# Optimization experiments

Hardware: AMD Instinct MI355X
Metric: run time of the kernel (lower is better)

## Reference

```python
import jax, jax.numpy as jnp
import numpy as np

B, N, D, H = 8, 1024, 1024, 16
HD = D // H  # head_size = 64


def setup_inputs() -> dict:
    key = jax.random.key(0)
    k0, k1, k2, k3, k4 = jax.random.split(key, 5)
    scale = 1.0 / np.sqrt(D)
    return {
        "x": jax.random.normal(k0, (B, N, D), dtype=jnp.float32),
        "Wqkv": jax.random.normal(k1, (D, 3 * D), dtype=jnp.float32) * scale,
        "bqkv": jnp.zeros((3 * D,), dtype=jnp.float32),
        "Wo": jax.random.normal(k2, (D, D), dtype=jnp.float32) * scale,
        "bo": jnp.zeros((D,), dtype=jnp.float32),
    }


def reference(x, Wqkv, bqkv, Wo, bo):
    # Fused QKV projection: [B, N, 3D]
    qkv = jnp.einsum("bnd,de->bne", x, Wqkv) + bqkv
    q, k, v = jnp.split(qkv, 3, axis=-1)

    def split_heads(t):  # [B, N, D] -> [B, H, N, HD]
        return t.reshape(B, N, H, HD).transpose(0, 2, 1, 3)

    q, k, v = split_heads(q), split_heads(k), split_heads(v)

    # Scaled dot-product attention (no mask, dropout=0)
    scores = jnp.einsum("bhqd,bhkd->bhqk", q, k) / jnp.sqrt(jnp.float32(HD))
    alpha = jax.nn.softmax(scores, axis=-1)
    ctx = jnp.einsum("bhqk,bhkd->bhqd", alpha, v)  # [B, H, N, HD]

    ctx = ctx.transpose(0, 2, 1, 3).reshape(B, N, D)
    out = jnp.einsum("bnd,de->bne", ctx, Wo) + bo
    return out
```

## Files before the change

kernel.cpp:

```cpp
#include <hip/hip_runtime.h>
#include <cstdint>
#include <cstddef>

typedef _Float16 half_t;
typedef __attribute__((ext_vector_type(4))) _Float16 half4v;
typedef __attribute__((ext_vector_type(8))) _Float16 half8v;
typedef __attribute__((ext_vector_type(4))) float float4v;
typedef __attribute__((ext_vector_type(16))) float float16v;
typedef __attribute__((ext_vector_type(4))) unsigned uint4v;
typedef __attribute__((ext_vector_type(2))) int int2v;

typedef __attribute__((address_space(1))) const void gv_t;
typedef __attribute__((address_space(3))) void lv_t;

__device__ __forceinline__ void lds_cp16(const void* g, void* l) {
  __builtin_amdgcn_global_load_lds((gv_t*)g, (lv_t*)l, 16, 0, 0);
}

__device__ __forceinline__ unsigned pkh(float a, float b) {
  return __builtin_bit_cast(unsigned, __builtin_amdgcn_cvt_pkrtz(a, b));
}

__global__ __launch_bounds__(256) void k_cvt(const float* __restrict__ in,
                                             half_t* __restrict__ out) {
  int i = blockIdx.x * 256 + threadIdx.x;
  float4 v = ((const float4*)in)[i];
  half4v h = {(half_t)v.x, (half_t)v.y, (half_t)v.z, (half_t)v.w};
  ((half4v*)out)[i] = h;
}

__global__ __launch_bounds__(256) void k_tcvt(const float* __restrict__ in,
                                              half_t* __restrict__ out, int R, int C) {
  __shared__ float t[32][33];
  int c0 = blockIdx.x * 32, r0 = blockIdx.y * 32;
  int tc = threadIdx.x & 31, tr = threadIdx.x >> 5;
#pragma unroll
  for (int i = 0; i < 4; i++)
    t[tr + i * 8][tc] = in[(size_t)(r0 + tr + i * 8) * C + c0 + tc];
  __syncthreads();
#pragma unroll
  for (int i = 0; i < 4; i++)
    out[(size_t)(c0 + tr + i * 8) * R + r0 + tc] = (half_t)t[tc][tr + i * 8];
}

template <int EPI>
__global__ __launch_bounds__(256, 2) void k_gemm(
    const half_t* __restrict__ A, const half_t* __restrict__ Bt,
    const float* __restrict__ bias, float* __restrict__ Cout,
    half_t* __restrict__ Qo, half_t* __restrict__ Ko, half_t* __restrict__ Vo,
    int M, int N, int K) {
  __shared__ half_t As[2][128 * 64];
  __shared__ half_t Bs[2][128 * 64];
  const int tid = threadIdx.x;
  const int lane = tid & 63;
  const int w = tid >> 6;
  const int xcd = blockIdx.x & 7;
  const int l = blockIdx.x >> 3;
  const int nc = l >> 6, r = l & 63;
  const int m0 = (xcd * 8 + (r >> 3)) * 128;
  const int n0 = (nc * 8 + (r & 7)) * 128;
  const int wr = w >> 1, wc = w & 1;

  int sr[4];
  int sg[4];
#pragma unroll
  for (int j = 0; j < 4; ++j) {
    const int G = j * 256 + tid;
    sr[j] = G >> 3;
    sg[j] = (G & 7) ^ (sr[j] & 7);
  }

  float4v acc[4][4] = {};

  const int fr = lane & 15;
  const int fg = lane >> 4;
  const int so0 = ((0 << 2) | fg) ^ (fr & 7);
  const int so1 = ((1 << 2) | fg) ^ (fr & 7);
  const int arow = wr * 64 + fr;
  const int brow = wc * 64 + fr;

  const int NT = K >> 6;
#pragma unroll
  for (int j = 0; j < 4; ++j) {
    lds_cp16(A + (size_t)(m0 + sr[j]) * K + sg[j] * 8, &As[0][(j * 256 + tid) * 8]);
    lds_cp16(Bt + (size_t)(n0 + sr[j]) * K + sg[j] * 8, &Bs[0][(j * 256 + tid) * 8]);
  }

  for (int t = 0; t < NT; t++) {
    asm volatile("s_waitcnt vmcnt(0)" ::: "memory");
    __builtin_amdgcn_s_barrier();
    __builtin_amdgcn_sched_barrier(0);
    const int cb = t & 1;
    if (t + 1 < NT) {
      const int kn = (t + 1) * 64;
#pragma unroll
      for (int j = 0; j < 4; ++j) {
        lds_cp16(A + (size_t)(m0 + sr[j]) * K + kn + sg[j] * 8,
                 &As[cb ^ 1][(j * 256 + tid) * 8]);
        lds_cp16(Bt + (size_t)(n0 + sr[j]) * K + kn + sg[j] * 8,
                 &Bs[cb ^ 1][(j * 256 + tid) * 8]);
      }
    }
    half8v a[4][2], b[4][2];
#pragma unroll
    for (int m = 0; m < 4; m++) {
      const int row = (arow + m * 16) * 64;
      a[m][0] = *(const half8v*)(&As[cb][row + so0 * 8]);
      a[m][1] = *(const half8v*)(&As[cb][row + so1 * 8]);
    }
#pragma unroll
    for (int n = 0; n < 4; n++) {
      const int row = (brow + n * 16) * 64;
      b[n][0] = *(const half8v*)(&Bs[cb][row + so0 * 8]);
      b[n][1] = *(const half8v*)(&Bs[cb][row + so1 * 8]);
    }
    __builtin_amdgcn_s_setprio(1);
#pragma unroll
    for (int kk = 0; kk < 2; kk++)
#pragma unroll
      for (int m = 0; m < 4; m++)
#pragma unroll
        for (int n = 0; n < 4; n++)
          acc[m][n] = __builtin_amdgcn_mfma_f32_16x16x32_f16(a[m][kk], b[n][kk],
                                                             acc[m][n], 0, 0, 0);
    __builtin_amdgcn_s_setprio(0);
  }

  const int rq = (lane >> 4) * 4;
  const int cc = lane & 15;
  if constexpr (EPI == 0) {
#pragma unroll
    for (int n = 0; n < 4; n++) {
      int e = n0 + wc * 64 + n * 16 + cc;
      float bv = bias[e];
      int which = e >> 10, h = (e >> 6) & 15, hd = e & 63;
#pragma unroll
      for (int m = 0; m < 4; m++) {
        int rowb = m0 + wr * 64 + m * 16 + rq;
#pragma unroll
        for (int r2 = 0; r2 < 4; r2++) {
          int row = rowb + r2;
          int b_ = row >> 10, tok = row & 1023;
          half_t hv = (half_t)(acc[m][n][r2] + bv);
          size_t bh = (size_t)(b_ * 16 + h);
          if (which == 0)
            Qo[(bh * 1024 + tok) * 64 + hd] = hv;
          else if (which == 1)
            Ko[(bh * 1024 + tok) * 64 + hd] = hv;
          else
            Vo[(bh * 64 + hd) * 1024 + tok] = hv;
        }
      }
    }
  } else {
#pragma unroll
    for (int n = 0; n < 4; n++) {
      int e = n0 + wc * 64 + n * 16 + cc;
      float bv = bias[e];
#pragma unroll
      for (int m = 0; m < 4; m++) {
        int rowb = m0 + wr * 64 + m * 16 + rq;
#pragma unroll
        for (int r2 = 0; r2 < 4; r2++)
          Cout[(size_t)(rowb + r2) * N + e] = acc[m][n][r2] + bv;
      }
    }
  }
}

__global__ __launch_bounds__(512, 4) void k_attn(const half_t* __restrict__ Qh,
                                                 const half_t* __restrict__ Kh,
                                                 const half_t* __restrict__ Vt,
                                                 half_t* __restrict__ ctx) {
  __shared__ alignas(16) half_t Ks[2][64 * 64];
  __shared__ alignas(16) half_t Vs[2][64 * 64];
  const int lane = threadIdx.x & 63;
  const int w = threadIdx.x >> 6;
  const int ql = lane & 31, hi = lane >> 5;
  const int xcd = blockIdx.x & 7, loc = blockIdx.x >> 3;
  const int bh = xcd * 16 + (loc >> 2), qb = loc & 3;
  const int b_ = bh >> 4, h = bh & 15;
  const int q0 = qb * 256 + w * 32;

  const half_t* Qp = Qh + (size_t)bh * (1024 * 64);
  const half_t* Kp = Kh + (size_t)bh * (1024 * 64);
  const half_t* Vp = Vt + (size_t)bh * (64 * 1024);

  half8v qf[4];
#pragma unroll
  for (int c = 0; c < 4; c++) {
    half8v tq = *(const half8v*)(Qp + (size_t)(q0 + ql) * 64 + c * 16 + hi * 8);
    qf[c] = tq * (_Float16)0.125f;
  }

  const int G = w * 64 + lane;
  const int rS = G >> 3;
  const int gS = (G & 7) ^ (rS & 7);

  float16v co[2] = {};
  float mr = -1e30f, ssum = 0.f;

  lds_cp16(Kp + (size_t)rS * 64 + gS * 8, &Ks[0][w * 512]);
  lds_cp16(Vp + (size_t)rS * 1024 + 0 + gS * 8, &Vs[0][w * 512]);
  __syncthreads();

  int cur = 0;
  for (int t = 0; t < 16; t++) {
    if (t < 15) {
      const int kn = (t + 1) * 64;
      lds_cp16(Kp + (size_t)(kn + rS) * 64 + gS * 8, &Ks[cur ^ 1][w * 512]);
      lds_cp16(Vp + (size_t)rS * 1024 + kn + gS * 8, &Vs[cur ^ 1][w * 512]);
    }

    float16v sacc[2] = {};
    __builtin_amdgcn_s_setprio(1);
#pragma unroll
    for (int c = 0; c < 4; c++)
#pragma unroll
      for (int s = 0; s < 2; s++) {
        int row = s * 32 + ql;
        half8v kf = *(const half8v*)(&Ks[cur][row * 64 + (((2 * c + hi) ^ (row & 7)) * 8)]);
        sacc[s] = __builtin_amdgcn_mfma_f32_32x32x16_f16(kf, qf[c], sacc[s], 0, 0, 0);
      }
    __builtin_amdgcn_s_setprio(0);

    float mx = -1e30f;
#pragma unroll
    for (int s = 0; s < 2; s++)
#pragma unroll
      for (int i = 0; i < 16; i++) mx = fmaxf(mx, sacc[s][i]);
    mx = fmaxf(mx, __shfl_xor(mx, 32, 64));
    if (mx > mr + 8.f) {
      float fac = __expf(mr - mx);
      mr = mx;
      ssum *= fac;
#pragma unroll
      for (int dd = 0; dd < 2; dd++)
#pragma unroll
        for (int i = 0; i < 16; i++) co[dd][i] *= fac;
    }
    float rsum = 0.f;
#pragma unroll
    for (int s = 0; s < 2; s++)
#pragma unroll
      for (int i = 0; i < 16; i++) {
        float e = __expf(sacc[s][i] - mr);
        sacc[s][i] = e;
        rsum += e;
      }
    rsum += __shfl_xor(rsum, 32, 64);
    ssum += rsum;

#pragma unroll
    for (int kc = 0; kc < 4; kc++) {
      const int s = kc >> 1, o = (kc & 1) * 8;
      unsigned dA0 = pkh(sacc[s][o + 0], sacc[s][o + 1]);
      unsigned dA1 = pkh(sacc[s][o + 2], sacc[s][o + 3]);
      unsigned dB0 = pkh(sacc[s][o + 4], sacc[s][o + 5]);
      unsigned dB1 = pkh(sacc[s][o + 6], sacc[s][o + 7]);
      int2v r0 = __builtin_amdgcn_permlane32_swap((int)dA0, (int)dB0, false, false);
      int2v r1 = __builtin_amdgcn_permlane32_swap((int)dA1, (int)dB1, false, false);
      uint4v pw = {(unsigned)r0.x, (unsigned)r1.x, (unsigned)r0.y, (unsigned)r1.y};
      half8v pf = __builtin_bit_cast(half8v, pw);
      __builtin_amdgcn_s_setprio(1);
#pragma unroll
      for (int dd = 0; dd < 2; dd++) {
        int row = dd * 32 + ql;
        half8v vf = *(const half8v*)(&Vs[cur][row * 64 + (((2 * kc + hi) ^ (row & 7)) * 8)]);
        co[dd] = __builtin_amdgcn_mfma_f32_32x32x16_f16(vf, pf, co[dd], 0, 0, 0);
      }
      __builtin_amdgcn_s_setprio(0);
    }
    __syncthreads();
    cur ^= 1;
  }

  float rinv = 1.0f / ssum;
  half_t* outp = ctx + ((size_t)(b_ * 1024 + q0 + ql) * 1024 + h * 64);
#pragma unroll
  for (int dd = 0; dd < 2; dd++)
#pragma unroll
    for (int g = 0; g < 4; g++) {
      int d0 = dd * 32 + g * 8 + hi * 4;
      unsigned p0 = pkh(co[dd][g * 4 + 0] * rinv, co[dd][g * 4 + 1] * rinv);
      unsigned p1 = pkh(co[dd][g * 4 + 2] * rinv, co[dd][g * 4 + 3] * rinv);
      *(unsigned*)(outp + d0) = p0;
      *(unsigned*)(outp + d0 + 2) = p1;
    }
}

extern "C" void kernel_launch(void* const* d_in, const int* in_sizes, int n_in,
                              void* d_out, int out_size, void* d_ws, size_t ws_size,
                              hipStream_t stream) {
  const float* x = (const float*)d_in[0];
  const float* Wqkv = (const float*)d_in[1];
  const float* bqkv = (const float*)d_in[2];
  const float* Wo = (const float*)d_in[3];
  const float* bo = (const float*)d_in[4];
  float* out = (float*)d_out;
  char* ws = (char*)d_ws;

  const size_t NEED = 75497472;
  if (ws_size < NEED) return;
  half_t* xh = (half_t*)(ws);
  half_t* wqkvT = (half_t*)(ws + 16777216);
  half_t* woT = (half_t*)(ws + 23068672);
  half_t* Qh = (half_t*)(ws + 25165824);
  half_t* Kh = (half_t*)(ws + 41943040);
  half_t* Vt = (half_t*)(ws + 58720256);
  half_t* ctxh = xh;

  k_cvt<<<8192, 256, 0, stream>>>(x, xh);
  k_tcvt<<<dim3(96, 32), 256, 0, stream>>>(Wqkv, wqkvT, 1024, 3072);
  k_tcvt<<<dim3(32, 32), 256, 0, stream>>>(Wo, woT, 1024, 1024);
  k_gemm<0><<<1536, 256, 0, stream>>>(xh, wqkvT, bqkv, nullptr, Qh, Kh, Vt,
                                      8192, 3072, 1024);
  k_attn<<<512, 512, 0, stream>>>(Qh, Kh, Vt, ctxh);
  k_gemm<1><<<512, 256, 0, stream>>>(ctxh, woT, bo, out, nullptr, nullptr, nullptr,
                                     8192, 1024, 1024);
}
```

Before: 171.3 us.

## Load QKV GEMM A operand directly to registers, halving LDS footprint

```diff
diff --git a/kernel.cpp b/kernel.cpp
--- a/kernel.cpp
+++ b/kernel.cpp
@@ -43,12 +43,111 @@
     out[(size_t)(c0 + tr + i * 8) * R + r0 + tc] = (half_t)t[tc][tr + i * 8];
 }
 
-template <int EPI>
-__global__ __launch_bounds__(256, 2) void k_gemm(
+__global__ __launch_bounds__(256, 3) void k_qkv(
     const half_t* __restrict__ A, const half_t* __restrict__ Bt,
-    const float* __restrict__ bias, float* __restrict__ Cout,
-    half_t* __restrict__ Qo, half_t* __restrict__ Ko, half_t* __restrict__ Vo,
-    int M, int N, int K) {
+    const float* __restrict__ bias,
+    half_t* __restrict__ Qo, half_t* __restrict__ Ko, half_t* __restrict__ Vo) {
+  __shared__ half_t Bs[2][128 * 64];
+  const int tid = threadIdx.x;
+  const int lane = tid & 63;
+  const int w = tid >> 6;
+  const int xcd = blockIdx.x & 7;
+  const int l = blockIdx.x >> 3;
+  const int nc = l >> 6, r = l & 63;
+  const int m0 = (xcd * 8 + (r >> 3)) * 128;
+  const int n0 = (nc * 8 + (r & 7)) * 128;
+  const int wr = w >> 1, wc = w & 1;
+  const int fr = lane & 15, fg = lane >> 4;
+
+  int sr[4], sg[4];
+#pragma unroll
+  for (int j = 0; j < 4; ++j) {
+    const int G = j * 256 + tid;
+    sr[j] = G >> 3;
+    sg[j] = (G & 7) ^ (sr[j] & 7);
+  }
+
+  const half_t* Ap = A + (size_t)(m0 + wr * 64 + fr) * 1024 + fg * 8;
+
+  float4v acc[4][4] = {};
+  const int so0 = fg ^ (fr & 7);
+  const int so1 = (4 | fg) ^ (fr & 7);
+  const int brow = wc * 64 + fr;
+
+  half8v a0[8], a1[8];
+#pragma unroll
+  for (int j = 0; j < 4; ++j)
+    lds_cp16(Bt + (size_t)(n0 + sr[j]) * 1024 + sg[j] * 8, &Bs[0][(j * 256 + tid) * 8]);
+#pragma unroll
+  for (int m = 0; m < 4; ++m)
+#pragma unroll
+    for (int kk = 0; kk < 2; ++kk)
+      a0[m * 2 + kk] = *(const half8v*)(Ap + m * 16384 + kk * 32);
+  asm volatile("s_waitcnt vmcnt(0)" ::: "memory");
+  __builtin_amdgcn_s_barrier();
+
+#define QKV_ITER(t, cb, ac, an)                                                  \
+  do {                                                                           \
+    if ((t) + 1 < 16) {                                                          \
+      const int kn = ((t) + 1) * 64;                                             \
+      _Pragma("unroll") for (int j = 0; j < 4; ++j)                              \
+          lds_cp16(Bt + (size_t)(n0 + sr[j]) * 1024 + kn + sg[j] * 8,            \
+                   &Bs[(cb) ^ 1][(j * 256 + tid) * 8]);                          \
+      _Pragma("unroll") for (int m = 0; m < 4; ++m)                              \
+          _Pragma("unroll") for (int kk = 0; kk < 2; ++kk)                       \
+              an[m * 2 + kk] = *(const half8v*)(Ap + m * 16384 + kn + kk * 32);  \
+    }                                                                            \
+    _Pragma("unroll") for (int kk = 0; kk < 2; ++kk) {                           \
+      half8v b[4];                                                               \
+      _Pragma("unroll") for (int n = 0; n < 4; ++n) {                            \
+        const int row = (brow + n * 16) * 64;                                    \
+        b[n] = *(const half8v*)(&Bs[cb][row + (kk ? so1 : so0) * 8]);            \
+      }                                                                          \
+      _Pragma("unroll") for (int m = 0; m < 4; ++m)                              \
+          _Pragma("unroll") for (int n = 0; n < 4; ++n)                          \
+              acc[m][n] = __builtin_amdgcn_mfma_f32_16x16x32_f16(                \
+                  ac[m * 2 + kk], b[n], acc[m][n], 0, 0, 0);                     \
+    }                                                                            \
+    asm volatile("s_waitcnt vmcnt(0)" ::: "memory");                             \
+    __builtin_amdgcn_s_barrier();                                                \
+  } while (0)
+
+  for (int tp = 0; tp < 8; ++tp) {
+    QKV_ITER(2 * tp, 0, a0, a1);
+    QKV_ITER(2 * tp + 1, 1, a1, a0);
+  }
+#undef QKV_ITER
+
+  const int rq = (lane >> 4) * 4;
+  const int cc = lane & 15;
+#pragma unroll
+  for (int n = 0; n < 4; n++) {
+    const int e = n0 + wc * 64 + n * 16 + cc;
+    const float bv = bias[e];
+    const int which = e >> 10, h = (e >> 6) & 15, hd = e & 63;
+#pragma unroll
+    for (int m = 0; m < 4; m++) {
+      const int rowb = m0 + wr * 64 + m * 16 + rq;
+#pragma unroll
+      for (int r2 = 0; r2 < 4; r2++) {
+        const int row = rowb + r2;
+        const int b_ = row >> 10, tok = row & 1023;
+        const half_t hv = (half_t)(acc[m][n][r2] + bv);
+        const size_t bh = (size_t)(b_ * 16 + h);
+        if (which == 0)
+          Qo[(bh * 1024 + tok) * 64 + hd] = hv;
+        else if (which == 1)
+          Ko[(bh * 1024 + tok) * 64 + hd] = hv;
+        else
+          Vo[(bh * 64 + hd) * 1024 + tok] = hv;
+      }
+    }
+  }
+}
+
+__global__ __launch_bounds__(256, 2) void k_gemm_o(
+    const half_t* __restrict__ A, const half_t* __restrict__ Bt,
+    const float* __restrict__ bias, float* __restrict__ Cout, int N, int K) {
   __shared__ half_t As[2][128 * 64];
   __shared__ half_t Bs[2][128 * 64];
   const int tid = threadIdx.x;
@@ -61,8 +160,7 @@
   const int n0 = (nc * 8 + (r & 7)) * 128;
   const int wr = w >> 1, wc = w & 1;
 
-  int sr[4];
-  int sg[4];
+  int sr[4], sg[4];
 #pragma unroll
   for (int j = 0; j < 4; ++j) {
     const int G = j * 256 + tid;
@@ -71,11 +169,10 @@
   }
 
   float4v acc[4][4] = {};
-
   const int fr = lane & 15;
   const int fg = lane >> 4;
-  const int so0 = ((0 << 2) | fg) ^ (fr & 7);
-  const int so1 = ((1 << 2) | fg) ^ (fr & 7);
+  const int so0 = fg ^ (fr & 7);
+  const int so1 = (4 | fg) ^ (fr & 7);
   const int arow = wr * 64 + fr;
   const int brow = wc * 64 + fr;
 
@@ -114,7 +211,6 @@
       b[n][0] = *(const half8v*)(&Bs[cb][row + so0 * 8]);
       b[n][1] = *(const half8v*)(&Bs[cb][row + so1 * 8]);
     }
-    __builtin_amdgcn_s_setprio(1);
 #pragma unroll
     for (int kk = 0; kk < 2; kk++)
 #pragma unroll
@@ -123,47 +219,20 @@
         for (int n = 0; n < 4; n++)
           acc[m][n] = __builtin_amdgcn_mfma_f32_16x16x32_f16(a[m][kk], b[n][kk],
                                                              acc[m][n], 0, 0, 0);
-    __builtin_amdgcn_s_setprio(0);
   }
 
   const int rq = (lane >> 4) * 4;
   const int cc = lane & 15;
-  if constexpr (EPI == 0) {
-#pragma unroll
-    for (int n = 0; n < 4; n++) {
-      int e = n0 + wc * 64 + n * 16 + cc;
-      float bv = bias[e];
-      int which = e >> 10, h = (e >> 6) & 15, hd = e & 63;
-#pragma unroll
-      for (int m = 0; m < 4; m++) {
-        int rowb = m0 + wr * 64 + m * 16 + rq;
-#pragma unroll
-        for (int r2 = 0; r2 < 4; r2++) {
-          int row = rowb + r2;
-          int b_ = row >> 10, tok = row & 1023;
-          half_t hv = (half_t)(acc[m][n][r2] + bv);
-          size_t bh = (size_t)(b_ * 16 + h);
-          if (which == 0)
-            Qo[(bh * 1024 + tok) * 64 + hd] = hv;
-          else if (which == 1)
-            Ko[(bh * 1024 + tok) * 64 + hd] = hv;
-          else
-            Vo[(bh * 64 + hd) * 1024 + tok] = hv;
-        }
-      }
-    }
-  } else {
-#pragma unroll
-    for (int n = 0; n < 4; n++) {
-      int e = n0 + wc * 64 + n * 16 + cc;
-      float bv = bias[e];
-#pragma unroll
-      for (int m = 0; m < 4; m++) {
-        int rowb = m0 + wr * 64 + m * 16 + rq;
-#pragma unroll
-        for (int r2 = 0; r2 < 4; r2++)
-          Cout[(size_t)(rowb + r2) * N + e] = acc[m][n][r2] + bv;
-      }
+#pragma unroll
+  for (int n = 0; n < 4; n++) {
+    int e = n0 + wc * 64 + n * 16 + cc;
+    float bv = bias[e];
+#pragma unroll
+    for (int m = 0; m < 4; m++) {
+      int rowb = m0 + wr * 64 + m * 16 + rq;
+#pragma unroll
+      for (int r2 = 0; r2 < 4; r2++)
+        Cout[(size_t)(rowb + r2) * N + e] = acc[m][n][r2] + bv;
     }
   }
 }
@@ -313,9 +382,7 @@
   k_cvt<<<8192, 256, 0, stream>>>(x, xh);
   k_tcvt<<<dim3(96, 32), 256, 0, stream>>>(Wqkv, wqkvT, 1024, 3072);
   k_tcvt<<<dim3(32, 32), 256, 0, stream>>>(Wo, woT, 1024, 1024);
-  k_gemm<0><<<1536, 256, 0, stream>>>(xh, wqkvT, bqkv, nullptr, Qh, Kh, Vt,
-                                      8192, 3072, 1024);
+  k_qkv<<<1536, 256, 0, stream>>>(xh, wqkvT, bqkv, Qh, Kh, Vt);
   k_attn<<<512, 512, 0, stream>>>(Qh, Kh, Vt, ctxh);
-  k_gemm<1><<<512, 256, 0, stream>>>(ctxh, woT, bo, out, nullptr, nullptr, nullptr,
-                                     8192, 1024, 1024);
-}
+  k_gemm_o<<<512, 256, 0, stream>>>(ctxh, woT, bo, out, 1024, 1024);
+}
```

Result: slower. 211.9 us (+23.7%).

## Process two 32-row query tiles per wave in attention to reuse K/V loads

Applied to the files above, without the earlier changes.

```diff
diff --git a/kernel.cpp b/kernel.cpp
--- a/kernel.cpp
+++ b/kernel.cpp
@@ -61,8 +61,7 @@
   const int n0 = (nc * 8 + (r & 7)) * 128;
   const int wr = w >> 1, wc = w & 1;
 
-  int sr[4];
-  int sg[4];
+  int sr[4], sg[4];
 #pragma unroll
   for (int j = 0; j < 4; ++j) {
     const int G = j * 256 + tid;
@@ -74,8 +73,8 @@
 
   const int fr = lane & 15;
   const int fg = lane >> 4;
-  const int so0 = ((0 << 2) | fg) ^ (fr & 7);
-  const int so1 = ((1 << 2) | fg) ^ (fr & 7);
+  const int so0 = fg ^ (fr & 7);
+  const int so1 = (4 | fg) ^ (fr & 7);
   const int arow = wr * 64 + fr;
   const int brow = wc * 64 + fr;
 
@@ -168,7 +167,7 @@
   }
 }
 
-__global__ __launch_bounds__(512, 4) void k_attn(const half_t* __restrict__ Qh,
+__global__ __launch_bounds__(512, 2) void k_attn(const half_t* __restrict__ Qh,
                                                  const half_t* __restrict__ Kh,
                                                  const half_t* __restrict__ Vt,
                                                  half_t* __restrict__ ctx) {
@@ -178,27 +177,31 @@
   const int w = threadIdx.x >> 6;
   const int ql = lane & 31, hi = lane >> 5;
   const int xcd = blockIdx.x & 7, loc = blockIdx.x >> 3;
-  const int bh = xcd * 16 + (loc >> 2), qb = loc & 3;
+  const int bh = xcd * 16 + (loc >> 1), qb = loc & 1;
   const int b_ = bh >> 4, h = bh & 15;
-  const int q0 = qb * 256 + w * 32;
+  const int q0 = qb * 512 + w * 64;
 
   const half_t* Qp = Qh + (size_t)bh * (1024 * 64);
   const half_t* Kp = Kh + (size_t)bh * (1024 * 64);
   const half_t* Vp = Vt + (size_t)bh * (64 * 1024);
 
-  half8v qf[4];
-#pragma unroll
-  for (int c = 0; c < 4; c++) {
-    half8v tq = *(const half8v*)(Qp + (size_t)(q0 + ql) * 64 + c * 16 + hi * 8);
-    qf[c] = tq * (_Float16)0.125f;
-  }
+  half8v qf[2][4];
+#pragma unroll
+  for (int u = 0; u < 2; u++)
+#pragma unroll
+    for (int c = 0; c < 4; c++) {
+      half8v tq =
+          *(const half8v*)(Qp + (size_t)(q0 + u * 32 + ql) * 64 + c * 16 + hi * 8);
+      qf[u][c] = tq * (_Float16)0.125f;
+    }
 
   const int G = w * 64 + lane;
   const int rS = G >> 3;
   const int gS = (G & 7) ^ (rS & 7);
 
-  float16v co[2] = {};
-  float mr = -1e30f, ssum = 0.f;
+  float16v co[2][2] = {};
+  float mr[2] = {-1e30f, -1e30f};
+  float ssum[2] = {};
 
   lds_cp16(Kp + (size_t)rS * 64 + gS * 8, &Ks[0][w * 512]);
   lds_cp16(Vp + (size_t)rS * 1024 + 0 + gS * 8, &Vs[0][w * 512]);
@@ -212,81 +215,89 @@
       lds_cp16(Vp + (size_t)rS * 1024 + kn + gS * 8, &Vs[cur ^ 1][w * 512]);
     }
 
-    float16v sacc[2] = {};
-    __builtin_amdgcn_s_setprio(1);
-#pragma unroll
-    for (int c = 0; c < 4; c++)
-#pragma unroll
-      for (int s = 0; s < 2; s++) {
-        int row = s * 32 + ql;
-        half8v kf = *(const half8v*)(&Ks[cur][row * 64 + (((2 * c + hi) ^ (row & 7)) * 8)]);
-        sacc[s] = __builtin_amdgcn_mfma_f32_32x32x16_f16(kf, qf[c], sacc[s], 0, 0, 0);
-      }
-    __builtin_amdgcn_s_setprio(0);
-
-    float mx = -1e30f;
-#pragma unroll
-    for (int s = 0; s < 2; s++)
-#pragma unroll
-      for (int i = 0; i < 16; i++) mx = fmaxf(mx, sacc[s][i]);
-    mx = fmaxf(mx, __shfl_xor(mx, 32, 64));
-    if (mx > mr + 8.f) {
-      float fac = __expf(mr - mx);
-      mr = mx;
-      ssum *= fac;
-#pragma unroll
-      for (int dd = 0; dd < 2; dd++)
-#pragma unroll
-        for (int i = 0; i < 16; i++) co[dd][i] *= fac;
-    }
-    float rsum = 0.f;
-#pragma unroll
-    for (int s = 0; s < 2; s++)
-#pragma unroll
-      for (int i = 0; i < 16; i++) {
-        float e = __expf(sacc[s][i] - mr);
-        sacc[s][i] = e;
-        rsum += e;
-      }
-    rsum += __shfl_xor(rsum, 32, 64);
-    ssum += rsum;
-
-#pragma unroll
-    for (int kc = 0; kc < 4; kc++) {
-      const int s = kc >> 1, o = (kc & 1) * 8;
-      unsigned dA0 = pkh(sacc[s][o + 0], sacc[s][o + 1]);
-      unsigned dA1 = pkh(sacc[s][o + 2], sacc[s][o + 3]);
-      unsigned dB0 = pkh(sacc[s][o + 4], sacc[s][o + 5]);
-      unsigned dB1 = pkh(sacc[s][o + 6], sacc[s][o + 7]);
-      int2v r0 = __builtin_amdgcn_permlane32_swap((int)dA0, (int)dB0, false, false);
-      int2v r1 = __builtin_amdgcn_permlane32_swap((int)dA1, (int)dB1, false, false);
-      uint4v pw = {(unsigned)r0.x, (unsigned)r1.x, (unsigned)r0.y, (unsigned)r1.y};
-      half8v pf = __builtin_bit_cast(half8v, pw);
+#pragma unroll
+    for (int u = 0; u < 2; u++) {
+      float16v sacc[2] = {};
       __builtin_amdgcn_s_setprio(1);
 #pragma unroll
-      for (int dd = 0; dd < 2; dd++) {
-        int row = dd * 32 + ql;
-        half8v vf = *(const half8v*)(&Vs[cur][row * 64 + (((2 * kc + hi) ^ (row & 7)) * 8)]);
-        co[dd] = __builtin_amdgcn_mfma_f32_32x32x16_f16(vf, pf, co[dd], 0, 0, 0);
-      }
+      for (int c = 0; c < 4; c++)
+#pragma unroll
+        for (int s = 0; s < 2; s++) {
+          int row = s * 32 + ql;
+          half8v kf =
+              *(const half8v*)(&Ks[cur][row * 64 + (((2 * c + hi) ^ (row & 7)) * 8)]);
+          sacc[s] = __builtin_amdgcn_mfma_f32_32x32x16_f16(kf, qf[u][c], sacc[s], 0, 0, 0);
+        }
       __builtin_amdgcn_s_setprio(0);
+
+      float mx = -1e30f;
+#pragma unroll
+      for (int s = 0; s < 2; s++)
+#pragma unroll
+        for (int i = 0; i < 16; i++) mx = fmaxf(mx, sacc[s][i]);
+      mx = fmaxf(mx, __shfl_xor(mx, 32, 64));
+      if (mx > mr[u] + 8.f) {
+        float fac = __expf(mr[u] - mx);
+        mr[u] = mx;
+        ssum[u] *= fac;
+#pragma unroll
+        for (int dd = 0; dd < 2; dd++)
+#pragma unroll
+          for (int i = 0; i < 16; i++) co[u][dd][i] *= fac;
+      }
+      float rsum = 0.f;
+#pragma unroll
+      for (int s = 0; s < 2; s++)
+#pragma unroll
+        for (int i = 0; i < 16; i++) {
+          float e = __expf(sacc[s][i] - mr[u]);
+          sacc[s][i] = e;
+          rsum += e;
+        }
+      rsum += __shfl_xor(rsum, 32, 64);
+      ssum[u] += rsum;
+
+#pragma unroll
+      for (int kc = 0; kc < 4; kc++) {
+        const int s = kc >> 1, o = (kc & 1) * 8;
+        unsigned dA0 = pkh(sacc[s][o + 0], sacc[s][o + 1]);
+        unsigned dA1 = pkh(sacc[s][o + 2], sacc[s][o + 3]);
+        unsigned dB0 = pkh(sacc[s][o + 4], sacc[s][o + 5]);
+        unsigned dB1 = pkh(sacc[s][o + 6], sacc[s][o + 7]);
+        int2v r0 = __builtin_amdgcn_permlane32_swap((int)dA0, (int)dB0, false, false);
+        int2v r1 = __builtin_amdgcn_permlane32_swap((int)dA1, (int)dB1, false, false);
+        uint4v pw = {(unsigned)r0.x, (unsigned)r1.x, (unsigned)r0.y, (unsigned)r1.y};
+        half8v pf = __builtin_bit_cast(half8v, pw);
+        __builtin_amdgcn_s_setprio(1);
+#pragma unroll
+        for (int dd = 0; dd < 2; dd++) {
+          int row = dd * 32 + ql;
+          half8v vf =
+              *(const half8v*)(&Vs[cur][row * 64 + (((2 * kc + hi) ^ (row & 7)) * 8)]);
+          co[u][dd] = __builtin_amdgcn_mfma_f32_32x32x16_f16(vf, pf, co[u][dd], 0, 0, 0);
+        }
+        __builtin_amdgcn_s_setprio(0);
+      }
     }
     __syncthreads();
     cur ^= 1;
   }
 
-  float rinv = 1.0f / ssum;
-  half_t* outp = ctx + ((size_t)(b_ * 1024 + q0 + ql) * 1024 + h * 64);
-#pragma unroll
-  for (int dd = 0; dd < 2; dd++)
-#pragma unroll
-    for (int g = 0; g < 4; g++) {
-      int d0 = dd * 32 + g * 8 + hi * 4;
-      unsigned p0 = pkh(co[dd][g * 4 + 0] * rinv, co[dd][g * 4 + 1] * rinv);
-      unsigned p1 = pkh(co[dd][g * 4 + 2] * rinv, co[dd][g * 4 + 3] * rinv);
-      *(unsigned*)(outp + d0) = p0;
-      *(unsigned*)(outp + d0 + 2) = p1;
-    }
+#pragma unroll
+  for (int u = 0; u < 2; u++) {
+    float rinv = 1.0f / ssum[u];
+    half_t* outp = ctx + ((size_t)(b_ * 1024 + q0 + u * 32 + ql) * 1024 + h * 64);
+#pragma unroll
+    for (int dd = 0; dd < 2; dd++)
+#pragma unroll
+      for (int g = 0; g < 4; g++) {
+        int d0 = dd * 32 + g * 8 + hi * 4;
+        unsigned p0 = pkh(co[u][dd][g * 4 + 0] * rinv, co[u][dd][g * 4 + 1] * rinv);
+        unsigned p1 = pkh(co[u][dd][g * 4 + 2] * rinv, co[u][dd][g * 4 + 3] * rinv);
+        *(unsigned*)(outp + d0) = p0;
+        *(unsigned*)(outp + d0 + 2) = p1;
+      }
+  }
 }
 
 extern "C" void kernel_launch(void* const* d_in, const int* in_sizes, int n_in,
@@ -315,7 +326,7 @@
   k_tcvt<<<dim3(32, 32), 256, 0, stream>>>(Wo, woT, 1024, 1024);
   k_gemm<0><<<1536, 256, 0, stream>>>(xh, wqkvT, bqkv, nullptr, Qh, Kh, Vt,
                                       8192, 3072, 1024);
-  k_attn<<<512, 512, 0, stream>>>(Qh, Kh, Vt, ctxh);
+  k_attn<<<256, 512, 0, stream>>>(Qh, Kh, Vt, ctxh);
   k_gemm<1><<<512, 256, 0, stream>>>(ctxh, woT, bo, out, nullptr, nullptr, nullptr,
                                      8192, 1024, 1024);
 }
```

New measurement: 175.0 us. 2.2% more time.
